# Optimization experiments

Hardware: AMD Instinct MI355X
Metric: run time of the kernel (lower is better)

The kernel has to match this reference:

```python
import jax, jax.numpy as jnp
import numpy as np

N_NODES = 100000
N_EDGES = 3200000
IN_FEATS = 128
OUT_FEATS = 16
NEG_SLOPE = 0.2


def setup_inputs() -> dict:
    key = jax.random.key(0)
    k1, k2, k3, k4, k5, k6 = jax.random.split(key, 6)
    h = jax.random.normal(k1, (N_NODES, IN_FEATS), dtype=jnp.float32)
    src = jax.random.randint(k2, (N_EDGES,), 0, N_NODES, dtype=jnp.int64)
    dst = jax.random.randint(k3, (N_EDGES,), 0, N_NODES, dtype=jnp.int64)
    W = jax.random.normal(k4, (OUT_FEATS, IN_FEATS), dtype=jnp.float32) * (1.0 / np.sqrt(IN_FEATS))
    a_l = jax.random.normal(k5, (1, OUT_FEATS), dtype=jnp.float32) * (1.0 / np.sqrt(OUT_FEATS))
    a_r = jax.random.normal(k6, (1, OUT_FEATS), dtype=jnp.float32) * (1.0 / np.sqrt(OUT_FEATS))
    return {"h": h, "src": src, "dst": dst, "W": W, "a_l": a_l, "a_r": a_r}


def reference(h, src, dst, W, a_l, a_r):
    N = h.shape[0]
    # node projection: h @ fc.weight.T  -> [N, out]
    hW = h @ W.T
    # per-node attention logits: [N, 1]
    el = hW @ a_l.T
    er = hW @ a_r.T
    # u_add_v: per-edge logit e = el[src] + er[dst], then leaky_relu(0.2)
    e = jax.nn.leaky_relu(el[src] + er[dst], negative_slope=NEG_SLOPE)  # [E, 1]
    # edge_softmax over edges grouped by destination node (numerically stable)
    emax = jax.ops.segment_max(e, dst, num_segments=N)  # [N, 1], -inf for empty
    emax = jnp.where(jnp.isfinite(emax), emax, 0.0)
    e_exp = jnp.exp(e - emax[dst])
    esum = jax.ops.segment_sum(e_exp, dst, num_segments=N)  # [N, 1]
    alpha = e_exp / jnp.maximum(esum[dst], 1e-16)  # [E, 1]
    # u_mul_e + sum: weighted aggregation of source features at destinations
    out = jax.ops.segment_sum(hW[src] * alpha, dst, num_segments=N)  # [N, out]
    return out
```

## Files before the change

### kernel.cpp

```cpp
#include <hip/hip_runtime.h>
#include <hip/hip_bf16.h>
#include <stdint.h>

#define IN_F 128
#define OUT_F 16
#define NEG_SLOPE 0.2f
#define LB_BITS 7
#define LB_NODES 128
#define NB 782
#define CAP 4608
#define SC_E 8192

#define SMEM_BYTES (12512 + 2048 + SC_E * 4)

__device__ __forceinline__ float u2f(uint32_t u) {
  union { uint32_t i; float f; } c;
  c.i = u;
  return c.f;
}

__global__ __launch_bounds__(512) void proj_scatter_kernel(
    const float* __restrict__ h, const float* __restrict__ W,
    const float* __restrict__ a_l, const float* __restrict__ a_r,
    const int* __restrict__ src, const int* __restrict__ dst,
    __hip_bfloat16* __restrict__ hWbf, float* __restrict__ el,
    float* __restrict__ er, int* __restrict__ cursor,
    uint32_t* __restrict__ payload, int N, int E, int scatBlocks) {
  __shared__ __align__(16) uint8_t smem[SMEM_BYTES];
  int t = threadIdx.x;

  if ((int)blockIdx.x < scatBlocks) {
    int* hist = (int*)smem;
    int* pref = hist + NB;
    int* gbase = pref + NB;
    int* rank = gbase + NB;
    int* tsum = rank + NB;
    uint32_t* sortedP = (uint32_t*)(tsum + 512);

    int start = blockIdx.x * SC_E;
    int end = min(E, start + SC_E);
    int cnt = end - start;

    for (int i = t; i < NB; i += 512) { hist[i] = 0; rank[i] = 0; }
    __syncthreads();

    const int4* d4 = (const int4*)(dst + start);
    int n4 = cnt >> 2;
    for (int i = t; i < n4; i += 512) {
      int4 d = d4[i];
      atomicAdd(&hist[d.x >> LB_BITS], 1);
      atomicAdd(&hist[d.y >> LB_BITS], 1);
      atomicAdd(&hist[d.z >> LB_BITS], 1);
      atomicAdd(&hist[d.w >> LB_BITS], 1);
    }
    for (int i = start + (n4 << 2) + t; i < end; i += 512)
      atomicAdd(&hist[dst[i] >> LB_BITS], 1);
    __syncthreads();

    {
      int b0 = t * 2;
      int s_loc = 0;
      if (b0 < NB) {
        int lim = min(b0 + 2, NB);
        for (int j = b0; j < lim; ++j) s_loc += hist[j];
      }
      tsum[t] = s_loc;
    }
    __syncthreads();
    {
      int pre = 0;
      for (int j = 0; j < t; ++j) pre += tsum[j];
      int b0 = t * 2;
      if (b0 < NB) {
        int lim = min(b0 + 2, NB);
        int run = pre;
        for (int j = b0; j < lim; ++j) {
          pref[j] = run;
          int c = hist[j];
          run += c;
          gbase[j] = c ? atomicAdd(&cursor[j * 16], c) : 0;
        }
      }
    }
    __syncthreads();

    const int4* s4 = (const int4*)(src + start);
    for (int i = t; i < n4; i += 512) {
      int4 d = d4[i];
      int4 s = s4[i];
#pragma unroll
      for (int j = 0; j < 4; ++j) {
        int dd = j == 0 ? d.x : j == 1 ? d.y : j == 2 ? d.z : d.w;
        int ss = j == 0 ? s.x : j == 1 ? s.y : j == 2 ? s.z : s.w;
        int b = dd >> LB_BITS;
        int r = atomicAdd(&rank[b], 1);
        sortedP[pref[b] + r] =
            ((uint32_t)ss << LB_BITS) | (uint32_t)(dd & (LB_NODES - 1));
      }
    }
    for (int i = start + (n4 << 2) + t; i < end; i += 512) {
      int dd = dst[i];
      int b = dd >> LB_BITS;
      int r = atomicAdd(&rank[b], 1);
      sortedP[pref[b] + r] =
          ((uint32_t)src[i] << LB_BITS) | (uint32_t)(dd & (LB_NODES - 1));
    }
    __syncthreads();

    int g16 = t >> 4, l16 = t & 15;
    for (int b = g16; b < NB; b += 32) {
      int c = hist[b];
      if (c == 0) continue;
      int p0 = pref[b];
      int gb = gbase[b];
      size_t g0 = (size_t)b * CAP + (size_t)gb;
      for (int j = l16; j < c; j += 16)
        if (gb + j < CAP) payload[g0 + j] = sortedP[p0 + j];
    }
  } else {
    float* Ws = (float*)smem;
    for (int i = t; i < OUT_F * IN_F; i += 512) Ws[i] = W[i];
    __syncthreads();

    int node = ((int)blockIdx.x - scatBlocks) * 512 + t;
    if (node >= N) return;

    const float4* hrow = (const float4*)(h + (size_t)node * IN_F);
    float acc[OUT_F];
#pragma unroll
    for (int f = 0; f < OUT_F; ++f) acc[f] = 0.f;

#pragma unroll 4
    for (int k = 0; k < IN_F / 4; ++k) {
      float4 hv = hrow[k];
#pragma unroll
      for (int f = 0; f < OUT_F; ++f) {
        float4 wv = ((const float4*)(Ws + f * IN_F))[k];
        acc[f] += hv.x * wv.x + hv.y * wv.y + hv.z * wv.z + hv.w * wv.w;
      }
    }

    union {
      unsigned short us[OUT_F];
      uint4 q[2];
    } pk;
#pragma unroll
    for (int f = 0; f < OUT_F; ++f) {
      __hip_bfloat16 b = __float2bfloat16(acc[f]);
      pk.us[f] = *reinterpret_cast<unsigned short*>(&b);
    }
    uint4* dstq = (uint4*)(hWbf + (size_t)node * OUT_F);
    dstq[0] = pk.q[0];
    dstq[1] = pk.q[1];

    float vl = 0.f, vr = 0.f;
#pragma unroll
    for (int f = 0; f < OUT_F; ++f) {
      vl += acc[f] * a_l[f];
      vr += acc[f] * a_r[f];
    }
    el[node] = vl;
    er[node] = vr;
  }
}

__global__ __launch_bounds__(512) void agg_kernel(
    const uint32_t* __restrict__ payload, const int* __restrict__ cursor,
    const __hip_bfloat16* __restrict__ hWbf, const float* __restrict__ el,
    const float* __restrict__ er, float* __restrict__ out, int N) {
  __shared__ __align__(16) uint2 pairs[CAP];
  __shared__ int hist[LB_NODES];
  __shared__ int pref[LB_NODES];
  __shared__ int rank[LB_NODES];
  __shared__ float erS[LB_NODES];

  int t = threadIdx.x;
  int b = blockIdx.x;
  size_t base = (size_t)b * CAP;
  int cnt = min(cursor[b * 16], CAP);
  int node0 = b << LB_BITS;

  if (t < LB_NODES) {
    hist[t] = 0;
    rank[t] = 0;
    int nd = node0 + t;
    erS[t] = nd < N ? er[nd] : 0.f;
  }
  __syncthreads();

  const uint4* pay4 = (const uint4*)(payload + base);
  int n4 = (cnt + 3) >> 2;
  for (int i = t; i < n4; i += 512) {
    uint4 v = pay4[i];
    int i0 = i << 2;
    if (i0 + 0 < cnt) atomicAdd(&hist[v.x & (LB_NODES - 1)], 1);
    if (i0 + 1 < cnt) atomicAdd(&hist[v.y & (LB_NODES - 1)], 1);
    if (i0 + 2 < cnt) atomicAdd(&hist[v.z & (LB_NODES - 1)], 1);
    if (i0 + 3 < cnt) atomicAdd(&hist[v.w & (LB_NODES - 1)], 1);
  }
  __syncthreads();

  if (t < LB_NODES) {
    int s = 0;
    for (int j = 0; j < t; ++j) s += hist[j];
    pref[t] = s;
  }
  __syncthreads();

  for (int i = t; i < cnt; i += 512) {
    uint32_t p = payload[base + i];
    int dl = (int)(p & (LB_NODES - 1));
    int r = atomicAdd(&rank[dl], 1);
    float x = el[p >> LB_BITS] + erS[dl];
    x = x > 0.f ? x : NEG_SLOPE * x;
    pairs[pref[dl] + r] = make_uint2(p, __float_as_uint(__expf(x)));
  }
  __syncthreads();

  int g = t >> 2, f4 = t & 3;
  int node = node0 + g;
  if (node < N) {
    int k = pref[g];
    int kend = k + hist[g];
    float a0 = 0.f, a1 = 0.f, a2 = 0.f, a3 = 0.f, es = 0.f;
    const uint2* hw2 = (const uint2*)hWbf;
#pragma unroll 4
    for (; k < kend; ++k) {
      uint2 q = pairs[k];
      float ex = __uint_as_float(q.y);
      uint2 w = hw2[(size_t)(q.x >> LB_BITS) * 4 + f4];
      a0 += ex * u2f(w.x << 16);
      a1 += ex * u2f(w.x & 0xffff0000u);
      a2 += ex * u2f(w.y << 16);
      a3 += ex * u2f(w.y & 0xffff0000u);
      es += ex;
    }
    float inv = 1.0f / fmaxf(es, 1e-16f);
    float4 o = make_float4(a0 * inv, a1 * inv, a2 * inv, a3 * inv);
    ((float4*)(out + (size_t)node * OUT_F))[f4] = o;
  }
}

extern "C" void kernel_launch(void* const* d_in, const int* in_sizes, int n_in,
                              void* d_out, int out_size, void* d_ws, size_t ws_size,
                              hipStream_t stream) {
  const float* h   = (const float*)d_in[0];
  const int*   src = (const int*)d_in[1];
  const int*   dst = (const int*)d_in[2];
  const float* W   = (const float*)d_in[3];
  const float* a_l = (const float*)d_in[4];
  const float* a_r = (const float*)d_in[5];
  float* out = (float*)d_out;

  const int N = in_sizes[0] / IN_F;
  const int E = in_sizes[1];
  const int scatBlocks = (E + SC_E - 1) / SC_E;
  const int projBlocks = (N + 511) / 512;

  __hip_bfloat16* hWbf = (__hip_bfloat16*)d_ws;
  float* el = (float*)(hWbf + (size_t)N * OUT_F);
  float* er = el + N;
  int* cursor = (int*)(er + N);
  uint32_t* payload = (uint32_t*)(cursor + (size_t)NB * 16);

  hipMemsetAsync(cursor, 0, (size_t)NB * 16 * sizeof(int), stream);

  proj_scatter_kernel<<<scatBlocks + projBlocks, 512, 0, stream>>>(
      h, W, a_l, a_r, src, dst, hWbf, el, er, cursor, payload, N, E, scatBlocks);

  agg_kernel<<<NB, 512, 0, stream>>>(payload, cursor, hWbf, el, er, out, N);
}
```

Baseline: 177.7 us.

## Scatter edge payloads directly to global buckets, dropping shared-memory staging sort

The scatter blocks no longer build a locally sorted copy of their edges in shared memory and then copy it out per bucket. After the histogram and global cursor reservation, each edge takes a slot with a shared atomic and writes its packed payload straight into global memory. This cuts shared memory from about 47KB to 8KB, which raises occupancy, and removes the prefix scan and the extra syncs. The cost is less coalesced global writes, since neighbouring threads now write to scattered buckets.

New measurement: 211.9 us. 19.2% more time.

```diff
diff --git a/kernel.cpp b/kernel.cpp
--- a/kernel.cpp
+++ b/kernel.cpp
@@ -11,7 +11,7 @@
 #define CAP 4608
 #define SC_E 8192
 
-#define SMEM_BYTES (12512 + 2048 + SC_E * 4)
+#define SMEM_BYTES 8192
 
 __device__ __forceinline__ float u2f(uint32_t u) {
   union { uint32_t i; float f; } c;
@@ -31,17 +31,13 @@
 
   if ((int)blockIdx.x < scatBlocks) {
     int* hist = (int*)smem;
-    int* pref = hist + NB;
-    int* gbase = pref + NB;
-    int* rank = gbase + NB;
-    int* tsum = rank + NB;
-    uint32_t* sortedP = (uint32_t*)(tsum + 512);
+    unsigned short* gbase = (unsigned short*)(smem + 3128);
 
     int start = blockIdx.x * SC_E;
     int end = min(E, start + SC_E);
     int cnt = end - start;
 
-    for (int i = t; i < NB; i += 512) { hist[i] = 0; rank[i] = 0; }
+    for (int i = t; i < NB; i += 512) hist[i] = 0;
     __syncthreads();
 
     const int4* d4 = (const int4*)(dst + start);
@@ -57,30 +53,11 @@
       atomicAdd(&hist[dst[i] >> LB_BITS], 1);
     __syncthreads();
 
-    {
-      int b0 = t * 2;
-      int s_loc = 0;
-      if (b0 < NB) {
-        int lim = min(b0 + 2, NB);
-        for (int j = b0; j < lim; ++j) s_loc += hist[j];
-      }
-      tsum[t] = s_loc;
-    }
-    __syncthreads();
-    {
-      int pre = 0;
-      for (int j = 0; j < t; ++j) pre += tsum[j];
-      int b0 = t * 2;
-      if (b0 < NB) {
-        int lim = min(b0 + 2, NB);
-        int run = pre;
-        for (int j = b0; j < lim; ++j) {
-          pref[j] = run;
-          int c = hist[j];
-          run += c;
-          gbase[j] = c ? atomicAdd(&cursor[j * 16], c) : 0;
-        }
-      }
+    for (int j = t; j < NB; j += 512) {
+      int c = hist[j];
+      int g = c ? atomicAdd(&cursor[j * 16], c) : 0;
+      gbase[j] = (unsigned short)min(g, CAP);
+      hist[j] = 0;
     }
     __syncthreads();
 
@@ -93,29 +70,19 @@
         int dd = j == 0 ? d.x : j == 1 ? d.y : j == 2 ? d.z : d.w;
         int ss = j == 0 ? s.x : j == 1 ? s.y : j == 2 ? s.z : s.w;
         int b = dd >> LB_BITS;
-        int r = atomicAdd(&rank[b], 1);
-        sortedP[pref[b] + r] =
-            ((uint32_t)ss << LB_BITS) | (uint32_t)(dd & (LB_NODES - 1));
+        int r = (int)gbase[b] + atomicAdd(&hist[b], 1);
+        if (r < CAP)
+          payload[(size_t)b * CAP + r] =
+              ((uint32_t)ss << LB_BITS) | (uint32_t)(dd & (LB_NODES - 1));
       }
     }
     for (int i = start + (n4 << 2) + t; i < end; i += 512) {
       int dd = dst[i];
       int b = dd >> LB_BITS;
-      int r = atomicAdd(&rank[b], 1);
-      sortedP[pref[b] + r] =
-          ((uint32_t)src[i] << LB_BITS) | (uint32_t)(dd & (LB_NODES - 1));
-    }
-    __syncthreads();
-
-    int g16 = t >> 4, l16 = t & 15;
-    for (int b = g16; b < NB; b += 32) {
-      int c = hist[b];
-      if (c == 0) continue;
-      int p0 = pref[b];
-      int gb = gbase[b];
-      size_t g0 = (size_t)b * CAP + (size_t)gb;
-      for (int j = l16; j < c; j += 16)
-        if (gb + j < CAP) payload[g0 + j] = sortedP[p0 + j];
+      int r = (int)gbase[b] + atomicAdd(&hist[b], 1);
+      if (r < CAP)
+        payload[(size_t)b * CAP + r] =
+            ((uint32_t)src[i] << LB_BITS) | (uint32_t)(dd & (LB_NODES - 1));
     }
   } else {
     float* Ws = (float*)smem;
```
